# Optimization experiments

Measured on AMD Instinct MI355X. Metric: run time of the kernel, lower is better.

Reference implementation:

```python
import jax, jax.numpy as jnp
import numpy as np
import math

B, N, C, H, CH = 4, 1024, 512, 8, 64  # batch, seq (Q=K), model dim, heads, head dim

def setup_inputs() -> dict:
    key = jax.random.key(0)
    ks = jax.random.split(key, 11)
    s = 0.02  # small init scale for weights
    f32 = jnp.float32
    return {
        "q_x": jax.random.normal(ks[0], (B, N, C), f32),
        "kv_x": jax.random.normal(ks[1], (B, N, C), f32),
        "bias_mask": jax.random.normal(ks[2], (B, 1, 1, N), f32),
        "bias_pair": jax.random.normal(ks[3], (1, H, N, N), f32),
        "Wq": (jax.random.normal(ks[4], (C, H * CH), f32) * s),
        "Wk": (jax.random.normal(ks[5], (C, H * CH), f32) * s),
        "Wv": (jax.random.normal(ks[6], (C, H * CH), f32) * s),
        "Wg": (jax.random.normal(ks[7], (C, H * CH), f32) * s),
        "bg": jnp.ones((H * CH,), f32),           # 'gating' init: bias=1
        "Wo": (jax.random.normal(ks[8], (H * CH, C), f32) * s),
        "bo": jnp.zeros((C,), f32),               # 'final' init
    }

def reference(q_x, kv_x, bias_mask, bias_pair, Wq, Wk, Wv, Wg, bg, Wo, bo):
    inv_sqrt = 1.0 / math.sqrt(CH)
    # projections -> [B, N, H, CH]
    q = (q_x @ Wq).reshape(B, N, H, CH) * inv_sqrt
    k = (kv_x @ Wk).reshape(B, N, H, CH)
    v = (kv_x @ Wv).reshape(B, N, H, CH)
    # scores [B, H, Q, K] with additive broadcast biases
    scores = jnp.einsum("bqhc,bkhc->bhqk", q, k) + bias_mask + bias_pair
    a = jax.nn.softmax(scores, axis=-1)
    o = jnp.einsum("bhqk,bkhc->bqhc", a, v)  # [B, Q, H, CH]
    # gated output
    g = jax.nn.sigmoid(q_x @ Wg + bg).reshape(B, N, H, CH)
    o = o * g
    out = o.reshape(B, N, H * CH) @ Wo + bo  # [B, Q, C]
    return out
```

## Files before the change

### kernel.cpp

```cpp
#include <hip/hip_runtime.h>
#include <hip/hip_bf16.h>
#include <hip/hip_fp16.h>

#define B_ 4
#define N_ 1024
#define C_ 512
#define H_ 8
#define CH_ 64

typedef _Float16 f16x8 __attribute__((ext_vector_type(8)));
typedef _Float16 f16x4 __attribute__((ext_vector_type(4)));
typedef float f32x4 __attribute__((ext_vector_type(4)));

__global__ void cvt_f32_f16(const float* __restrict__ xq, const float* __restrict__ xkv,
                            _Float16* __restrict__ oq, _Float16* __restrict__ okv) {
  const int n4 = (B_ * N_ * C_) / 4;
  int stride = gridDim.x * blockDim.x;
  for (int idx = blockIdx.x * blockDim.x + threadIdx.x; idx < 2 * n4; idx += stride) {
    const float4* src = (idx < n4) ? (const float4*)xq : (const float4*)xkv;
    _Float16* dst = (idx < n4) ? oq : okv;
    int j = (idx < n4) ? idx : idx - n4;
    float4 v = src[j];
    f16x4 h;
    h[0] = (_Float16)v.x; h[1] = (_Float16)v.y;
    h[2] = (_Float16)v.z; h[3] = (_Float16)v.w;
    *(f16x4*)(dst + (size_t)j * 4) = h;
  }
}

__global__ void transpose_w(const float* __restrict__ Wq, const float* __restrict__ Wk,
                            const float* __restrict__ Wv, const float* __restrict__ Wg,
                            const float* __restrict__ Wo, _Float16* __restrict__ WT) {
  int s = blockIdx.z;
  const float* W = (s == 0) ? Wq : (s == 1) ? Wk : (s == 2) ? Wv : (s == 3) ? Wg : Wo;
  __shared__ float tile[32][33];
  int tx = threadIdx.x & 31, ty = threadIdx.x >> 5;
  int k0 = blockIdx.x * 32, n0 = blockIdx.y * 32;
  #pragma unroll
  for (int r = 0; r < 32; r += 8)
    tile[ty + r][tx] = W[(size_t)(k0 + ty + r) * C_ + n0 + tx];
  __syncthreads();
  _Float16* dst = WT + (size_t)s * C_ * C_;
  #pragma unroll
  for (int r = 0; r < 32; r += 8)
    dst[(size_t)(n0 + ty + r) * C_ + k0 + tx] = (_Float16)tile[tx][ty + r];
}

__global__ __launch_bounds__(256, 2) void proj_gemm(
    const _Float16* __restrict__ xq16, const _Float16* __restrict__ xkv16,
    const _Float16* __restrict__ WT, const float* __restrict__ bg,
    _Float16* __restrict__ Qb, _Float16* __restrict__ Kh,
    _Float16* __restrict__ Vt, _Float16* __restrict__ Gb) {
  int nt0 = blockIdx.x * 128;
  int m0 = blockIdx.y * 128;
  int sel = nt0 >> 9;
  int n0 = nt0 & 511;
  const _Float16* X = (sel == 0 || sel == 3) ? xq16 : xkv16;
  const _Float16* Wt = WT + (size_t)sel * C_ * C_;

  __shared__ __align__(16) char lds[32768];
  char* ldsA = lds;
  char* ldsB = lds + 16384;

  int tid = threadIdx.x;
  int lane = tid & 63, w = tid >> 6;
  int wr = w >> 1, wc = w & 1;
  int lr = lane & 15, lg = lane >> 4;

  f32x4 acc[4][4];
  #pragma unroll
  for (int i = 0; i < 4; i++)
    #pragma unroll
    for (int j = 0; j < 4; j++)
      #pragma unroll
      for (int r = 0; r < 4; r++) acc[i][j][r] = 0.f;

  int srow = tid >> 3, scol = tid & 7;

  for (int k0 = 0; k0 < C_; k0 += 64) {
    __syncthreads();
    #pragma unroll
    for (int p = 0; p < 4; p++) {
      int r = p * 32 + srow;
      *(f16x8*)(ldsA + ((r * 128 + scol * 16) ^ ((r & 7) << 4))) =
          *(const f16x8*)(X + (size_t)(m0 + r) * C_ + k0 + scol * 8);
      *(f16x8*)(ldsB + ((r * 128 + scol * 16) ^ ((r & 7) << 4))) =
          *(const f16x8*)(Wt + (size_t)(n0 + r) * C_ + k0 + scol * 8);
    }
    __syncthreads();
    #pragma unroll
    for (int kh = 0; kh < 2; kh++) {
      f16x8 a[4], b[4];
      #pragma unroll
      for (int i = 0; i < 4; i++) {
        int row = wr * 64 + i * 16 + lr;
        a[i] = *(const f16x8*)(ldsA + ((row * 128 + kh * 64 + lg * 16) ^ ((row & 7) << 4)));
        int col = wc * 64 + i * 16 + lr;
        b[i] = *(const f16x8*)(ldsB + ((col * 128 + kh * 64 + lg * 16) ^ ((col & 7) << 4)));
      }
      #pragma unroll
      for (int i = 0; i < 4; i++)
        #pragma unroll
        for (int j = 0; j < 4; j++)
          acc[i][j] = __builtin_amdgcn_mfma_f32_16x16x32_f16(a[i], b[j], acc[i][j], 0, 0, 0);
    }
  }

  const float inv_sqrt = 0.125f;
  #pragma unroll
  for (int i = 0; i < 4; i++) {
    int token = m0 + wr * 64 + i * 16 + lg * 4;
    #pragma unroll
    for (int j = 0; j < 4; j++) {
      int col = n0 + wc * 64 + j * 16 + lr;
      f32x4 v = acc[i][j];
      if (sel == 0) {
        #pragma unroll
        for (int r = 0; r < 4; r++)
          Qb[(size_t)(token + r) * C_ + col] = (_Float16)(v[r] * inv_sqrt);
      } else if (sel == 1) {
        int bb = token >> 10, nn = token & 1023;
        int hh = col >> 6, ch = col & 63;
        #pragma unroll
        for (int r = 0; r < 4; r++)
          Kh[((size_t)(hh * B_ + bb) * N_ + nn + r) * CH_ + ch] = (_Float16)v[r];
      } else if (sel == 2) {
        int bb = token >> 10, nn = token & 1023;
        int hh = col >> 6, ch = col & 63;
        f16x4 pk;
        #pragma unroll
        for (int r = 0; r < 4; r++) pk[r] = (_Float16)v[r];
        *(f16x4*)(Vt + ((size_t)((bb * H_ + hh) * CH_) + ch) * N_ + nn) = pk;
      } else {
        #pragma unroll
        for (int r = 0; r < 4; r++) {
          float x = v[r] + bg[col];
          Gb[(size_t)(token + r) * C_ + col] = (_Float16)(1.f / (1.f + __expf(-x)));
        }
      }
    }
  }
}

__global__ __launch_bounds__(256) void attn(
    const _Float16* __restrict__ Qb, const _Float16* __restrict__ Kh,
    const _Float16* __restrict__ Vt, const _Float16* __restrict__ Gb,
    const float* __restrict__ bias_mask, const float* __restrict__ bias_pair,
    _Float16* __restrict__ Ob) {
  int bid = blockIdx.x;
  int h = bid & 7, b = (bid >> 3) & 3, qt = bid >> 5;
  int q0 = qt * 64;
  int tid = threadIdx.x, lane = tid & 63, w = tid >> 6;
  int lr = lane & 15, lg = lane >> 4;

  __shared__ __align__(16) char lds[32768];
  char* ldsK = lds;
  char* ldsV = lds + 16384;

  f16x8 qf[2];
  {
    const _Float16* qp = Qb + (size_t)(b * N_ + q0 + w * 16 + lr) * C_ + h * CH_;
    qf[0] = *(const f16x8*)(qp + lg * 8);
    qf[1] = *(const f16x8*)(qp + 32 + lg * 8);
  }

  f32x4 acc_o[4];
  #pragma unroll
  for (int j = 0; j < 4; j++)
    #pragma unroll
    for (int r = 0; r < 4; r++) acc_o[j][r] = 0.f;
  float m_run = -1e30f, l_run = 0.f;

  int srow = tid >> 3, scol = tid & 7;
  int vrow = tid >> 4, vcol = tid & 15;

  const _Float16* Kbase = Kh + (size_t)((h * B_ + b) * N_) * CH_;
  const _Float16* Vbase = Vt + (size_t)((b * H_ + h) * CH_) * N_;
  const float* bpbase = bias_pair + ((size_t)h * N_ + q0 + w * 16 + lr) * N_ + lg * 4;
  const float* bmbase = bias_mask + b * N_ + lg * 4;

  f16x8 kr[4], vr[4];
  #pragma unroll
  for (int pp = 0; pp < 4; pp++) {
    kr[pp] = *(const f16x8*)(Kbase + (size_t)(pp * 32 + srow) * CH_ + scol * 8);
    vr[pp] = *(const f16x8*)(Vbase + (size_t)(pp * 16 + vrow) * N_ + vcol * 8);
  }
  f32x4 bp_c[8];
  #pragma unroll
  for (int ct = 0; ct < 8; ct++) bp_c[ct] = *(const f32x4*)(bpbase + ct * 16);

  for (int kt = 0; kt < 8; kt++) {
    __syncthreads();
    #pragma unroll
    for (int pp = 0; pp < 4; pp++) {
      int r = pp * 32 + srow;
      *(f16x8*)(ldsK + ((r * 128 + scol * 16) ^ ((r & 7) << 4))) = kr[pp];
      int rv = pp * 16 + vrow;
      *(f16x8*)(ldsV + ((rv * 256 + vcol * 16) ^ ((rv & 7) << 4))) = vr[pp];
    }
    __syncthreads();
    if (kt < 7) {
      #pragma unroll
      for (int pp = 0; pp < 4; pp++) {
        kr[pp] = *(const f16x8*)(Kbase + (size_t)((kt + 1) * 128 + pp * 32 + srow) * CH_ + scol * 8);
        vr[pp] = *(const f16x8*)(Vbase + (size_t)(pp * 16 + vrow) * N_ + (kt + 1) * 128 + vcol * 8);
      }
    }
    f32x4 s[8];
    #pragma unroll
    for (int ct = 0; ct < 8; ct++)
      s[ct] = bp_c[ct] + *(const f32x4*)(bmbase + kt * 128 + ct * 16);
    if (kt < 7) {
      #pragma unroll
      for (int ct = 0; ct < 8; ct++)
        bp_c[ct] = *(const f32x4*)(bpbase + (kt + 1) * 128 + ct * 16);
    }
    #pragma unroll
    for (int ct = 0; ct < 8; ct++) {
      #pragma unroll
      for (int kh = 0; kh < 2; kh++) {
        int row = ct * 16 + lr;
        f16x8 kf = *(const f16x8*)(ldsK + ((row * 128 + kh * 64 + lg * 16) ^ ((row & 7) << 4)));
        s[ct] = __builtin_amdgcn_mfma_f32_16x16x32_f16(kf, qf[kh], s[ct], 0, 0, 0);
      }
    }
    float mx = s[0][0];
    #pragma unroll
    for (int ct = 0; ct < 8; ct++)
      #pragma unroll
      for (int r = 0; r < 4; r++) mx = fmaxf(mx, s[ct][r]);
    mx = fmaxf(mx, __shfl_xor(mx, 16, 64));
    mx = fmaxf(mx, __shfl_xor(mx, 32, 64));
    float m_new = fmaxf(m_run, mx);
    float sc = __expf(m_run - m_new);
    m_run = m_new;
    float sum = 0.f;
    #pragma unroll
    for (int ct = 0; ct < 8; ct++)
      #pragma unroll
      for (int r = 0; r < 4; r++) {
        float pv = __expf(s[ct][r] - m_new);
        s[ct][r] = pv;
        sum += pv;
      }
    sum += __shfl_xor(sum, 16, 64);
    sum += __shfl_xor(sum, 32, 64);
    l_run = l_run * sc + sum;
    #pragma unroll
    for (int j = 0; j < 4; j++)
      #pragma unroll
      for (int r = 0; r < 4; r++) acc_o[j][r] *= sc;
    #pragma unroll
    for (int ct = 0; ct < 8; ct++) {
      f16x4 pf;
      #pragma unroll
      for (int r = 0; r < 4; r++) pf[r] = (_Float16)s[ct][r];
      #pragma unroll
      for (int cc = 0; cc < 4; cc++) {
        int vrr = cc * 16 + lr;
        f16x4 vf = *(const f16x4*)(ldsV + ((vrr * 256 + ct * 32 + lg * 8) ^ ((vrr & 7) << 4)));
        acc_o[cc] = __builtin_amdgcn_mfma_f32_16x16x16f16(vf, pf, acc_o[cc], 0, 0, 0);
      }
    }
  }

  {
    int token = b * N_ + q0 + w * 16 + lr;
    float inv_l = 1.f / l_run;
    #pragma unroll
    for (int cc = 0; cc < 4; cc++) {
      int col = h * CH_ + cc * 16 + lg * 4;
      f16x4 g4 = *(const f16x4*)(Gb + (size_t)token * C_ + col);
      f16x4 o4;
      #pragma unroll
      for (int r = 0; r < 4; r++)
        o4[r] = (_Float16)(acc_o[cc][r] * inv_l * (float)g4[r]);
      *(f16x4*)(Ob + (size_t)token * C_ + col) = o4;
    }
  }
}

__global__ __launch_bounds__(256, 2) void out_gemm(
    const _Float16* __restrict__ Ob, const _Float16* __restrict__ WTo,
    const float* __restrict__ bo, float* __restrict__ out) {
  int n0 = blockIdx.x * 128;
  int m0 = blockIdx.y * 128;
  __shared__ __align__(16) char lds[32768];
  char* ldsA = lds;
  char* ldsB = lds + 16384;
  int tid = threadIdx.x;
  int lane = tid & 63, w = tid >> 6;
  int wr = w >> 1, wc = w & 1;
  int lr = lane & 15, lg = lane >> 4;
  f32x4 acc[4][4];
  #pragma unroll
  for (int i = 0; i < 4; i++)
    #pragma unroll
    for (int j = 0; j < 4; j++)
      #pragma unroll
      for (int r = 0; r < 4; r++) acc[i][j][r] = 0.f;
  int srow = tid >> 3, scol = tid & 7;
  for (int k0 = 0; k0 < C_; k0 += 64) {
    __syncthreads();
    #pragma unroll
    for (int p = 0; p < 4; p++) {
      int r = p * 32 + srow;
      *(f16x8*)(ldsA + ((r * 128 + scol * 16) ^ ((r & 7) << 4))) =
          *(const f16x8*)(Ob + (size_t)(m0 + r) * C_ + k0 + scol * 8);
      *(f16x8*)(ldsB + ((r * 128 + scol * 16) ^ ((r & 7) << 4))) =
          *(const f16x8*)(WTo + (size_t)(n0 + r) * C_ + k0 + scol * 8);
    }
    __syncthreads();
    #pragma unroll
    for (int kh = 0; kh < 2; kh++) {
      f16x8 a[4], bfr[4];
      #pragma unroll
      for (int i = 0; i < 4; i++) {
        int row = wr * 64 + i * 16 + lr;
        a[i] = *(const f16x8*)(ldsA + ((row * 128 + kh * 64 + lg * 16) ^ ((row & 7) << 4)));
        int col = wc * 64 + i * 16 + lr;
        bfr[i] = *(const f16x8*)(ldsB + ((col * 128 + kh * 64 + lg * 16) ^ ((col & 7) << 4)));
      }
      #pragma unroll
      for (int i = 0; i < 4; i++)
        #pragma unroll
        for (int j = 0; j < 4; j++)
          acc[i][j] = __builtin_amdgcn_mfma_f32_16x16x32_f16(a[i], bfr[j], acc[i][j], 0, 0, 0);
    }
  }
  #pragma unroll
  for (int i = 0; i < 4; i++) {
    int token = m0 + wr * 64 + i * 16 + lg * 4;
    #pragma unroll
    for (int j = 0; j < 4; j++) {
      int col = n0 + wc * 64 + j * 16 + lr;
      float bb = bo[col];
      #pragma unroll
      for (int r = 0; r < 4; r++)
        out[(size_t)(token + r) * C_ + col] = acc[i][j][r] + bb;
    }
  }
}

extern "C" void kernel_launch(void* const* d_in, const int* in_sizes, int n_in,
                              void* d_out, int out_size, void* d_ws, size_t ws_size,
                              hipStream_t stream) {
  const float* q_x = (const float*)d_in[0];
  const float* kv_x = (const float*)d_in[1];
  const float* bias_mask = (const float*)d_in[2];
  const float* bias_pair = (const float*)d_in[3];
  const float* Wq = (const float*)d_in[4];
  const float* Wk = (const float*)d_in[5];
  const float* Wv = (const float*)d_in[6];
  const float* Wg = (const float*)d_in[7];
  const float* bg = (const float*)d_in[8];
  const float* Wo = (const float*)d_in[9];
  const float* bo = (const float*)d_in[10];
  float* out = (float*)d_out;

  char* ws = (char*)d_ws;
  const size_t MB = 1024 * 1024;
  _Float16* xq16 = (_Float16*)(ws + 0);
  _Float16* xkv16 = (_Float16*)(ws + 4 * MB);
  _Float16* WT = (_Float16*)(ws + 8 * MB);
  _Float16* Qb = (_Float16*)(ws + 11 * MB);
  _Float16* Kh = (_Float16*)(ws + 15 * MB);
  _Float16* Vt = (_Float16*)(ws + 19 * MB);
  _Float16* Gb = (_Float16*)(ws + 23 * MB);
  _Float16* Ob = (_Float16*)(ws + 27 * MB);

  cvt_f32_f16<<<2048, 256, 0, stream>>>(q_x, kv_x, xq16, xkv16);
  transpose_w<<<dim3(16, 16, 5), 256, 0, stream>>>(Wq, Wk, Wv, Wg, Wo, WT);
  proj_gemm<<<dim3(16, 32), 256, 0, stream>>>(xq16, xkv16, WT, bg, Qb, Kh, Vt, Gb);
  attn<<<512, 256, 0, stream>>>(Qb, Kh, Vt, Gb, bias_mask, bias_pair, Ob);
  out_gemm<<<dim3(4, 32), 256, 0, stream>>>(Ob, WT + 4 * (size_t)C_ * C_, bo, out);
}
```

Before: 80.19 us.

## Fuse input f32-to-f16 conversion into projection GEMM and tighten softmax

Removes the separate cvt_f32_f16 kernel. The projection GEMM now loads fp32 activations and converts them to fp16 while staging into LDS, which saves a launch and a full write-and-read of the fp16 copies. The attention kernel gets launch_bounds(256,2), a tree-shaped max reduction, and a fused exp/pack path using cvt_pkrtz with the row sum moved after the PV MFMAs. In exchange, each GEMM tile re-reads and re-converts fp32 inputs, which doubles the A-operand bytes per tile, and round-toward-zero packing slightly changes precision.

```diff
diff --git a/kernel.cpp b/kernel.cpp
--- a/kernel.cpp
+++ b/kernel.cpp
@@ -10,23 +10,8 @@
 
 typedef _Float16 f16x8 __attribute__((ext_vector_type(8)));
 typedef _Float16 f16x4 __attribute__((ext_vector_type(4)));
+typedef __fp16 fp16x2 __attribute__((ext_vector_type(2)));
 typedef float f32x4 __attribute__((ext_vector_type(4)));
-
-__global__ void cvt_f32_f16(const float* __restrict__ xq, const float* __restrict__ xkv,
-                            _Float16* __restrict__ oq, _Float16* __restrict__ okv) {
-  const int n4 = (B_ * N_ * C_) / 4;
-  int stride = gridDim.x * blockDim.x;
-  for (int idx = blockIdx.x * blockDim.x + threadIdx.x; idx < 2 * n4; idx += stride) {
-    const float4* src = (idx < n4) ? (const float4*)xq : (const float4*)xkv;
-    _Float16* dst = (idx < n4) ? oq : okv;
-    int j = (idx < n4) ? idx : idx - n4;
-    float4 v = src[j];
-    f16x4 h;
-    h[0] = (_Float16)v.x; h[1] = (_Float16)v.y;
-    h[2] = (_Float16)v.z; h[3] = (_Float16)v.w;
-    *(f16x4*)(dst + (size_t)j * 4) = h;
-  }
-}
 
 __global__ void transpose_w(const float* __restrict__ Wq, const float* __restrict__ Wk,
                             const float* __restrict__ Wv, const float* __restrict__ Wg,
@@ -47,7 +32,7 @@
 }
 
 __global__ __launch_bounds__(256, 2) void proj_gemm(
-    const _Float16* __restrict__ xq16, const _Float16* __restrict__ xkv16,
+    const float* __restrict__ xq, const float* __restrict__ xkv,
     const _Float16* __restrict__ WT, const float* __restrict__ bg,
     _Float16* __restrict__ Qb, _Float16* __restrict__ Kh,
     _Float16* __restrict__ Vt, _Float16* __restrict__ Gb) {
@@ -55,7 +40,7 @@
   int m0 = blockIdx.y * 128;
   int sel = nt0 >> 9;
   int n0 = nt0 & 511;
-  const _Float16* X = (sel == 0 || sel == 3) ? xq16 : xkv16;
+  const float* X = (sel == 0 || sel == 3) ? xq : xkv;
   const _Float16* Wt = WT + (size_t)sel * C_ * C_;
 
   __shared__ __align__(16) char lds[32768];
@@ -82,8 +67,15 @@
     #pragma unroll
     for (int p = 0; p < 4; p++) {
       int r = p * 32 + srow;
-      *(f16x8*)(ldsA + ((r * 128 + scol * 16) ^ ((r & 7) << 4))) =
-          *(const f16x8*)(X + (size_t)(m0 + r) * C_ + k0 + scol * 8);
+      const float* xp = X + (size_t)(m0 + r) * C_ + k0 + scol * 8;
+      float4 a0 = *(const float4*)xp;
+      float4 a1 = *(const float4*)(xp + 4);
+      f16x8 hx;
+      hx[0] = (_Float16)a0.x; hx[1] = (_Float16)a0.y;
+      hx[2] = (_Float16)a0.z; hx[3] = (_Float16)a0.w;
+      hx[4] = (_Float16)a1.x; hx[5] = (_Float16)a1.y;
+      hx[6] = (_Float16)a1.z; hx[7] = (_Float16)a1.w;
+      *(f16x8*)(ldsA + ((r * 128 + scol * 16) ^ ((r & 7) << 4))) = hx;
       *(f16x8*)(ldsB + ((r * 128 + scol * 16) ^ ((r & 7) << 4))) =
           *(const f16x8*)(Wt + (size_t)(n0 + r) * C_ + k0 + scol * 8);
     }
@@ -142,7 +134,7 @@
   }
 }
 
-__global__ __launch_bounds__(256) void attn(
+__global__ __launch_bounds__(256, 2) void attn(
     const _Float16* __restrict__ Qb, const _Float16* __restrict__ Kh,
     const _Float16* __restrict__ Vt, const _Float16* __restrict__ Gb,
     const float* __restrict__ bias_mask, const float* __restrict__ bias_pair,
@@ -224,37 +216,34 @@
         s[ct] = __builtin_amdgcn_mfma_f32_16x16x32_f16(kf, qf[kh], s[ct], 0, 0, 0);
       }
     }
-    float mx = s[0][0];
+    float t[8];
     #pragma unroll
     for (int ct = 0; ct < 8; ct++)
-      #pragma unroll
-      for (int r = 0; r < 4; r++) mx = fmaxf(mx, s[ct][r]);
+      t[ct] = fmaxf(fmaxf(s[ct][0], s[ct][1]), fmaxf(s[ct][2], s[ct][3]));
+    float mx = fmaxf(fmaxf(fmaxf(t[0], t[1]), fmaxf(t[2], t[3])),
+                     fmaxf(fmaxf(t[4], t[5]), fmaxf(t[6], t[7])));
     mx = fmaxf(mx, __shfl_xor(mx, 16, 64));
     mx = fmaxf(mx, __shfl_xor(mx, 32, 64));
     float m_new = fmaxf(m_run, mx);
     float sc = __expf(m_run - m_new);
     m_run = m_new;
-    float sum = 0.f;
-    #pragma unroll
-    for (int ct = 0; ct < 8; ct++)
-      #pragma unroll
-      for (int r = 0; r < 4; r++) {
-        float pv = __expf(s[ct][r] - m_new);
-        s[ct][r] = pv;
-        sum += pv;
-      }
-    sum += __shfl_xor(sum, 16, 64);
-    sum += __shfl_xor(sum, 32, 64);
-    l_run = l_run * sc + sum;
     #pragma unroll
     for (int j = 0; j < 4; j++)
       #pragma unroll
       for (int r = 0; r < 4; r++) acc_o[j][r] *= sc;
+    float psum[8];
     #pragma unroll
     for (int ct = 0; ct < 8; ct++) {
+      float p0 = __expf(s[ct][0] - m_new);
+      float p1 = __expf(s[ct][1] - m_new);
+      float p2 = __expf(s[ct][2] - m_new);
+      float p3 = __expf(s[ct][3] - m_new);
+      psum[ct] = (p0 + p1) + (p2 + p3);
+      fp16x2 lo = __builtin_amdgcn_cvt_pkrtz(p0, p1);
+      fp16x2 hi = __builtin_amdgcn_cvt_pkrtz(p2, p3);
       f16x4 pf;
-      #pragma unroll
-      for (int r = 0; r < 4; r++) pf[r] = (_Float16)s[ct][r];
+      pf[0] = (_Float16)lo[0]; pf[1] = (_Float16)lo[1];
+      pf[2] = (_Float16)hi[0]; pf[3] = (_Float16)hi[1];
       #pragma unroll
       for (int cc = 0; cc < 4; cc++) {
         int vrr = cc * 16 + lr;
@@ -262,6 +251,11 @@
         acc_o[cc] = __builtin_amdgcn_mfma_f32_16x16x16f16(vf, pf, acc_o[cc], 0, 0, 0);
       }
     }
+    float sum = ((psum[0] + psum[1]) + (psum[2] + psum[3])) +
+                ((psum[4] + psum[5]) + (psum[6] + psum[7]));
+    sum += __shfl_xor(sum, 16, 64);
+    sum += __shfl_xor(sum, 32, 64);
+    l_run = l_run * sc + sum;
   }
 
   {
@@ -360,18 +354,15 @@
 
   char* ws = (char*)d_ws;
   const size_t MB = 1024 * 1024;
-  _Float16* xq16 = (_Float16*)(ws + 0);
-  _Float16* xkv16 = (_Float16*)(ws + 4 * MB);
-  _Float16* WT = (_Float16*)(ws + 8 * MB);
-  _Float16* Qb = (_Float16*)(ws + 11 * MB);
-  _Float16* Kh = (_Float16*)(ws + 15 * MB);
-  _Float16* Vt = (_Float16*)(ws + 19 * MB);
-  _Float16* Gb = (_Float16*)(ws + 23 * MB);
-  _Float16* Ob = (_Float16*)(ws + 27 * MB);
-
-  cvt_f32_f16<<<2048, 256, 0, stream>>>(q_x, kv_x, xq16, xkv16);
+  _Float16* WT = (_Float16*)(ws + 0);
+  _Float16* Qb = (_Float16*)(ws + 3 * MB);
+  _Float16* Kh = (_Float16*)(ws + 7 * MB);
+  _Float16* Vt = (_Float16*)(ws + 11 * MB);
+  _Float16* Gb = (_Float16*)(ws + 15 * MB);
+  _Float16* Ob = (_Float16*)(ws + 19 * MB);
+
   transpose_w<<<dim3(16, 16, 5), 256, 0, stream>>>(Wq, Wk, Wv, Wg, Wo, WT);
-  proj_gemm<<<dim3(16, 32), 256, 0, stream>>>(xq16, xkv16, WT, bg, Qb, Kh, Vt, Gb);
+  proj_gemm<<<dim3(16, 32), 256, 0, stream>>>(q_x, kv_x, WT, bg, Qb, Kh, Vt, Gb);
   attn<<<512, 256, 0, stream>>>(Qb, Kh, Vt, Gb, bias_mask, bias_pair, Ob);
   out_gemm<<<dim3(4, 32), 256, 0, stream>>>(Ob, WT + 4 * (size_t)C_ * C_, bo, out);
 }
```

New measurement: 84.73 us. 5.7% more time.
